# Kernel tuning notes

Hardware: AMD Instinct MI355X
Metric: run time of the kernel (lower is better)

The kernel has to match this reference:

```python
import jax, jax.numpy as jnp
import numpy as np

B, L, K, D = 8, 4096, 16, 128


def setup_inputs() -> dict:
    key = jax.random.key(0)
    k1, k2 = jax.random.split(key)
    frame = jax.random.normal(k1, (B, L, 4, 3), dtype=jnp.float32)  # [B,L,4,3]: row0=center, rows1-3=frame axes
    attr = jax.random.normal(k2, (B, L, D), dtype=jnp.float32)
    return {"frame": frame, "attr": attr}


def reference(frame, attr):
    Kmax = 16
    center = frame[:, :, 0]  # [B,L,3]
    # pairwise squared distances (no grad needed through topk selection)
    c_ng = jax.lax.stop_gradient(center)
    diff = c_ng[:, :, None, :] - c_ng[:, None, :, :]  # [B,L,L,3]
    distance_sq = jnp.sum(diff * diff, axis=-1)  # [B,L,L]
    # k nearest neighbors (smallest distance)
    _, nbr = jax.lax.top_k(-distance_sq, Kmax)  # [B,L,K] int32 indices
    # gather neighbor attributes: attr[b, nbr[b,l,k], :]
    gathered_attr = jax.vmap(lambda a, i: a[i])(attr, nbr)  # [B,L,K,D]
    # gather neighbor centers and project delta into local frame
    nbr_center = jax.vmap(lambda c, i: c[i])(center, nbr)  # [B,L,K,3]
    delta = nbr_center - center[:, :, None, :]  # [B,L,K,3]
    euclidian = jnp.einsum('blkc,blcr->blkr', delta, frame[:, :, 1:4])  # [B,L,K,3]
    return (euclidian, gathered_attr)
```

## Files before the change

### kernel.cpp

```cpp
#include <hip/hip_runtime.h>
#include <stdint.h>

typedef unsigned long long u64;
typedef unsigned short u16;
typedef float nfloat4 __attribute__((ext_vector_type(4)));

#define LQ   4096
#define BQ   8
#define KNB  16
#define TPB  512
#define QPB  64
#define BPB  (LQ / QPB)

__device__ __forceinline__ void ceu(uint32_t &a, uint32_t &b) {
    const uint32_t mn = a < b ? a : b;
    const uint32_t mx = a < b ? b : a;
    a = mn; b = mx;
}
__device__ __forceinline__ void ced(double &a, double &b) {
    const double mn = __builtin_fmin(a, b);
    const double mx = __builtin_fmax(a, b);
    a = mn; b = mx;
}
__device__ __forceinline__ float dist2(float mx, float my, float mz,
                                       float px, float py, float pz) {
    const float dx = __fsub_rn(mx, px);
    const float dy = __fsub_rn(my, py);
    const float dz = __fsub_rn(mz, pz);
    return __fadd_rn(__fadd_rn(__fmul_rn(dx, dx), __fmul_rn(dy, dy)),
                     __fmul_rn(dz, dz));
}

__global__ __launch_bounds__(512) void sort_kernel(
    const float4* __restrict__ frame4,
    float* __restrict__ wx, float* __restrict__ wy,
    float* __restrict__ wz, int* __restrict__ wperm)
{
    __shared__ u64 SK[LQ];
    const int b   = blockIdx.x;
    const int tid = threadIdx.x;
    const float4* fb = frame4 + (size_t)b * LQ * 3;

    for (int j = tid; j < LQ; j += 512) {
        const uint32_t bits = __float_as_uint(fb[j * 3].x);
        const uint32_t mk = (bits & 0x80000000u) ? ~bits : (bits | 0x80000000u);
        SK[j] = ((u64)mk << 32) | (unsigned)j;
    }
    __syncthreads();
    for (int k = 2; k <= LQ; k <<= 1) {
        for (int g = k >> 1; g >= 1; g >>= 1) {
            for (int t = tid; t < LQ / 2; t += 512) {
                const int i  = ((t & ~(g - 1)) << 1) | (t & (g - 1));
                const int j2 = i | g;
                const bool up = ((i & k) == 0);
                const u64 a = SK[i], c = SK[j2];
                if ((a > c) == up) { SK[i] = c; SK[j2] = a; }
            }
            __syncthreads();
        }
    }
    for (int p = tid; p < LQ; p += 512) {
        const int orig = (int)(SK[p] & 0xFFFu);
        const float4 v = fb[orig * 3];
        const size_t o = (size_t)b * LQ + p;
        wx[o] = v.x; wy[o] = v.y; wz[o] = v.z; wperm[o] = orig;
    }
}


__global__ __launch_bounds__(TPB) void knn_fused_kernel(
    const float4* __restrict__ frame4,
    const float4* __restrict__ attr4,
    const float* __restrict__ wx, const float* __restrict__ wy,
    const float* __restrict__ wz, const int* __restrict__ wperm,
    float* __restrict__ out_e,
    nfloat4* __restrict__ outg4)
{
    __shared__ float xs[LQ], ys[LQ], zs[LQ];
    __shared__ u16 perm_lds[LQ];
    __shared__ u16 inv_lds[LQ];
    __shared__ u16 surv[QPB][32];
    __shared__ int nbrs[QPB][KNB];

    const int b    = blockIdx.x >> 6;
    const int qblk = blockIdx.x & (BPB - 1);
    const int tid  = threadIdx.x;

    const float4* fb = frame4 + (size_t)b * LQ * 3;
    {
        const float* bx = wx + (size_t)b * LQ;
        const float* by = wy + (size_t)b * LQ;
        const float* bz = wz + (size_t)b * LQ;
        const int*   bp = wperm + (size_t)b * LQ;
        for (int j = tid; j < LQ; j += TPB) {
            xs[j] = bx[j]; ys[j] = by[j]; zs[j] = bz[j];
            const int pm = bp[j];
            perm_lds[j] = (u16)pm;
            inv_lds[pm] = (u16)j;
        }
    }
    __syncthreads();

    const int qloc = tid >> 3;
    const int h    = tid & 7;
    const int wv   = tid >> 6;
    const int l    = qblk * QPB + qloc;
    const float mx = xs[l], my = ys[l], mz = zs[l];
    const float xq_lo = xs[qblk * QPB + wv * 8];
    const float xq_hi = xs[qblk * QPB + wv * 8 + 7];

    uint32_t R[16];
#pragma unroll
    for (int i = 0; i < 16; ++i) R[i] = 0xFFFFFFFFu;

    const int A = qblk * QPB;
    int lo = A, hi = A;
    bool doneR = false;
    bool doneL = (lo <= 0);

#pragma unroll 1
    while (!(doneR && doneL)) {
        int base;
        {
            bool goRight;
            if (doneR) goRight = false;
            else if (doneL) goRight = true;
            else {
                const float dR = __fsub_rn(xs[hi], xq_hi);
                const float dL = __fsub_rn(xq_lo, xs[lo - 1]);
                goRight = !(dR > dL);
            }
            if (goRight) { base = hi; hi += 64; }
            else         { lo -= 64; base = lo; }
        }
        uint32_t K[8];
#pragma unroll
        for (int s = 0; s < 8; ++s) {
            const int pos = base + s * 8 + h;
            const int pp  = pos < 0 ? 0 : pos;
            const float dx = __fsub_rn(mx, xs[pp]);
            const float dy = __fsub_rn(my, ys[pp]);
            const float dz = __fsub_rn(mz, zs[pp]);
            const float d  = __fmaf_rn(dz, dz, __fmaf_rn(dy, dy, __fmul_rn(dx, dx)));
            const uint32_t key = (__float_as_uint(d) & 0xFFFFF000u) | (unsigned)pos;
            K[s] = (pos >= 0) ? key : 0xFFFFFFFFu;
        }
        ceu(K[0],K[1]); ceu(K[2],K[3]); ceu(K[4],K[5]); ceu(K[6],K[7]);
        ceu(K[0],K[2]); ceu(K[1],K[3]); ceu(K[4],K[6]); ceu(K[5],K[7]);
        ceu(K[1],K[2]); ceu(K[5],K[6]);
        ceu(K[0],K[4]); ceu(K[1],K[5]); ceu(K[2],K[6]); ceu(K[3],K[7]);
        ceu(K[2],K[4]); ceu(K[3],K[5]);
        ceu(K[1],K[2]); ceu(K[3],K[4]); ceu(K[5],K[6]);
#pragma unroll
        for (int t = 0; t < 8; ++t) {
            const uint32_t x = R[8 + t], y = K[7 - t];
            R[8 + t] = x < y ? x : y;
        }
#pragma unroll
        for (int g = 8; g >= 1; g >>= 1)
#pragma unroll
            for (int i = 0; i < 16; ++i)
                if ((i & g) == 0) ceu(R[i], R[i + g]);

        uint32_t ub = R[15] | 0xFFFu;
        { uint32_t t;
          t = __shfl_xor(ub, 1, 64); ub = ub < t ? ub : t;
          t = __shfl_xor(ub, 2, 64); ub = ub < t ? ub : t;
          t = __shfl_xor(ub, 4, 64); ub = ub < t ? ub : t; }
        uint32_t ubb = (ub & 0xFFFFF000u) | 0xFFFu;
        ubb = ubb >> 12;
        ubb = (ubb << 12) | 0xFFFu;
        ubb = (ubb > 0xFFFFFFEFu) ? 0xFFFFFFFFu : ubb + 16u;

        if (!doneR) {
            if (hi >= LQ) doneR = true;
            else {
                const float dxm = __fsub_rn(xs[hi], mx);
                const bool st = (dxm > 0.f) &&
                                (__float_as_uint(__fmul_rn(dxm, dxm)) > ubb);
                if (__all(st)) doneR = true;
            }
        }
        if (!doneL) {
            if (lo <= 0) doneL = true;
            else {
                const float dxm = __fsub_rn(mx, xs[lo - 1]);
                const bool st = (dxm > 0.f) &&
                                (__float_as_uint(__fmul_rn(dxm, dxm)) > ubb);
                if (__all(st)) doneL = true;
            }
        }
    }

    {
        uint32_t P[16];
#pragma unroll
        for (int i = 0; i < 16; ++i) P[i] = __shfl_xor(R[i], 1, 64);
        const bool lo1 = (h & 1) == 0;
#pragma unroll
        for (int i = 0; i < 16; ++i) {
            const uint32_t o = P[15 - i];
            R[i] = lo1 ? (R[i] < o ? R[i] : o) : (R[i] > o ? R[i] : o);
        }
#pragma unroll
        for (int g = 8; g >= 1; g >>= 1)
#pragma unroll
            for (int i = 0; i < 16; ++i)
                if ((i & g) == 0) ceu(R[i], R[i + g]);
    }
    {
        uint32_t P[16];
#pragma unroll
        for (int i = 0; i < 16; ++i) P[i] = __shfl_xor(R[i], 3, 64);
        const bool lo2 = (h & 2) == 0;
#pragma unroll
        for (int i = 0; i < 16; ++i) {
            const uint32_t o = P[15 - i];
            R[i] = lo2 ? (R[i] < o ? R[i] : o) : (R[i] > o ? R[i] : o);
        }
#pragma unroll
        for (int i = 0; i < 16; ++i) P[i] = __shfl_xor(R[i], 1, 64);
        const bool lo1 = (h & 1) == 0;
#pragma unroll
        for (int i = 0; i < 16; ++i) {
            const uint32_t o = P[i];
            R[i] = lo1 ? (R[i] < o ? R[i] : o) : (R[i] > o ? R[i] : o);
        }
#pragma unroll
        for (int g = 8; g >= 1; g >>= 1)
#pragma unroll
            for (int i = 0; i < 16; ++i)
                if ((i & g) == 0) ceu(R[i], R[i + g]);
    }
    {
        uint32_t P[16];
#pragma unroll
        for (int i = 0; i < 16; ++i) P[i] = __shfl_xor(R[i], 7, 64);
        const bool lo4 = (h & 4) == 0;
#pragma unroll
        for (int i = 0; i < 16; ++i) {
            const uint32_t o = P[15 - i];
            R[i] = lo4 ? (R[i] < o ? R[i] : o) : (R[i] > o ? R[i] : o);
        }
#pragma unroll
        for (int i = 0; i < 16; ++i) P[i] = __shfl_xor(R[i], 2, 64);
        const bool lo2 = (h & 2) == 0;
#pragma unroll
        for (int i = 0; i < 16; ++i) {
            const uint32_t o = P[i];
            R[i] = lo2 ? (R[i] < o ? R[i] : o) : (R[i] > o ? R[i] : o);
        }
#pragma unroll
        for (int i = 0; i < 16; ++i) P[i] = __shfl_xor(R[i], 1, 64);
        const bool lo1 = (h & 1) == 0;
#pragma unroll
        for (int i = 0; i < 16; ++i) {
            const uint32_t o = P[i];
            R[i] = lo1 ? (R[i] < o ? R[i] : o) : (R[i] > o ? R[i] : o);
        }
#pragma unroll
        for (int g = 8; g >= 1; g >>= 1)
#pragma unroll
            for (int i = 0; i < 16; ++i)
                if ((i & g) == 0) ceu(R[i], R[i + g]);
    }

    if (h < 2) {
#pragma unroll
        for (int i = 0; i < 16; ++i)
            surv[qloc][h * 16 + i] = (u16)(R[i] & 0xFFFu);
    }

    double kd[4];
#pragma unroll
    for (int s = 0; s < 4; ++s) {
        const int sp = surv[qloc][h * 4 + s];
        const float d = dist2(mx, my, mz, xs[sp], ys[sp], zs[sp]);
        kd[s] = __builtin_bit_cast(double,
                 ((u64)__float_as_uint(d) << 12) | (unsigned)perm_lds[sp]);
    }
    ced(kd[0],kd[1]); ced(kd[2],kd[3]); ced(kd[0],kd[2]); ced(kd[1],kd[3]); ced(kd[1],kd[2]);
    {
        double P[4];
#pragma unroll
        for (int s = 0; s < 4; ++s) P[s] = __shfl_xor(kd[s], 1, 64);
        const bool lo1 = (h & 1) == 0;
#pragma unroll
        for (int s = 0; s < 4; ++s) {
            const double o = P[3 - s];
            kd[s] = lo1 ? __builtin_fmin(kd[s], o) : __builtin_fmax(kd[s], o);
        }
        ced(kd[0],kd[2]); ced(kd[1],kd[3]); ced(kd[0],kd[1]); ced(kd[2],kd[3]);
    }
    {
        double P[4];
#pragma unroll
        for (int s = 0; s < 4; ++s) P[s] = __shfl_xor(kd[s], 3, 64);
        const bool lo2 = (h & 2) == 0;
#pragma unroll
        for (int s = 0; s < 4; ++s) {
            const double o = P[3 - s];
            kd[s] = lo2 ? __builtin_fmin(kd[s], o) : __builtin_fmax(kd[s], o);
        }
#pragma unroll
        for (int s = 0; s < 4; ++s) P[s] = __shfl_xor(kd[s], 1, 64);
        const bool lo1 = (h & 1) == 0;
#pragma unroll
        for (int s = 0; s < 4; ++s) {
            const double o = P[s];
            kd[s] = lo1 ? __builtin_fmin(kd[s], o) : __builtin_fmax(kd[s], o);
        }
        ced(kd[0],kd[2]); ced(kd[1],kd[3]); ced(kd[0],kd[1]); ced(kd[2],kd[3]);
    }
    {
        double P[4];
#pragma unroll
        for (int s = 0; s < 4; ++s) P[s] = __shfl_xor(kd[s], 7, 64);
        const bool lo4 = (h & 4) == 0;
#pragma unroll
        for (int s = 0; s < 4; ++s) {
            const double o = P[3 - s];
            kd[s] = lo4 ? __builtin_fmin(kd[s], o) : __builtin_fmax(kd[s], o);
        }
#pragma unroll
        for (int s = 0; s < 4; ++s) P[s] = __shfl_xor(kd[s], 2, 64);
        const bool lo2 = (h & 2) == 0;
#pragma unroll
        for (int s = 0; s < 4; ++s) {
            const double o = P[s];
            kd[s] = lo2 ? __builtin_fmin(kd[s], o) : __builtin_fmax(kd[s], o);
        }
#pragma unroll
        for (int s = 0; s < 4; ++s) P[s] = __shfl_xor(kd[s], 1, 64);
        const bool lo1 = (h & 1) == 0;
#pragma unroll
        for (int s = 0; s < 4; ++s) {
            const double o = P[s];
            kd[s] = lo1 ? __builtin_fmin(kd[s], o) : __builtin_fmax(kd[s], o);
        }
        ced(kd[0],kd[2]); ced(kd[1],kd[3]); ced(kd[0],kd[1]); ced(kd[2],kd[3]);
    }

    const int ql_orig = perm_lds[l];
    const size_t gq = (size_t)b * LQ + (size_t)ql_orig;
    if (h < 4) {
        const float4 f0 = fb[ql_orig * 3 + 0];
        const float4 f1 = fb[ql_orig * 3 + 1];
        const float4 f2 = fb[ql_orig * 3 + 2];
        const float R00 = f0.w, R01 = f1.x, R02 = f1.y;
        const float R10 = f1.z, R11 = f1.w, R12 = f2.x;
        const float R20 = f2.y, R21 = f2.z, R22 = f2.w;
        float e[12];
#pragma unroll
        for (int s = 0; s < 4; ++s) {
            const u64 bits = __builtin_bit_cast(u64, kd[s]);
            const int jo = (int)(bits & 0xFFFu);
            nbrs[qloc][h * 4 + s] = jo;
            const int sp = inv_lds[jo];
            const float dx = xs[sp] - mx;
            const float dy = ys[sp] - my;
            const float dz = zs[sp] - mz;
            e[s * 3 + 0] = dx * R00 + dy * R10 + dz * R20;
            e[s * 3 + 1] = dx * R01 + dy * R11 + dz * R21;
            e[s * 3 + 2] = dx * R02 + dy * R12 + dz * R22;
        }
        float4* eo = (float4*)(out_e + gq * 48 + h * 12);
        float4 v0 = {e[0], e[1], e[2],  e[3]};
        float4 v1 = {e[4], e[5], e[6],  e[7]};
        float4 v2 = {e[8], e[9], e[10], e[11]};
        eo[0] = v0; eo[1] = v1; eo[2] = v2;
    }

    const float4* ab = attr4 + (((size_t)b) << 12) * 32;
    const int lane = tid & 63;
    const int qbase = qblk * QPB + wv * 8;
#pragma unroll 4
    for (int it = 0; it < 64; ++it) {
        const int idx = it * 64 + lane;
        const int qw  = idx >> 9;
        const int r   = idx & 511;
        const int k   = r >> 5, d4 = r & 31;
        const int nb  = nbrs[wv * 8 + qw][k];
        const int qo  = perm_lds[qbase + qw];
        const float4 v = ab[(size_t)nb * 32 + d4];
        nfloat4 nv = {v.x, v.y, v.z, v.w};
        __builtin_nontemporal_store(nv,
            &outg4[((size_t)b * LQ + (size_t)qo) * 512 + r]);
    }
}

extern "C" void kernel_launch(void* const* d_in, const int* in_sizes, int n_in,
                              void* d_out, int out_size, void* d_ws, size_t ws_size,
                              hipStream_t stream)
{
    const float* frame = (const float*)d_in[0];
    const float* attr  = (const float*)d_in[1];
    float* out = (float*)d_out;

    float* wxp = (float*)d_ws;
    float* wyp = wxp + BQ * LQ;
    float* wzp = wyp + BQ * LQ;
    int*   wpp = (int*)(wzp + BQ * LQ);

    sort_kernel<<<BQ, 512, 0, stream>>>((const float4*)frame, wxp, wyp, wzp, wpp);

    nfloat4* outg4 = (nfloat4*)(out + (size_t)BQ * LQ * KNB * 3);
    knn_fused_kernel<<<BQ * BPB, TPB, 0, stream>>>(
        (const float4*)frame, (const float4*)attr, wxp, wyp, wzp, wpp,
        out, outg4);
}
```

Baseline: 396.8 us.

## Replace adaptive bidirectional kNN scan with seeded radius bound and binary-searched window

New measurement: 372.5 us. 6.1% less time.

```diff
diff --git a/kernel.cpp b/kernel.cpp
--- a/kernel.cpp
+++ b/kernel.cpp
@@ -106,44 +106,21 @@
     const int wv   = tid >> 6;
     const int l    = qblk * QPB + qloc;
     const float mx = xs[l], my = ys[l], mz = zs[l];
-    const float xq_lo = xs[qblk * QPB + wv * 8];
-    const float xq_hi = xs[qblk * QPB + wv * 8 + 7];
 
     uint32_t R[16];
 #pragma unroll
     for (int i = 0; i < 16; ++i) R[i] = 0xFFFFFFFFu;
 
-    const int A = qblk * QPB;
-    int lo = A, hi = A;
-    bool doneR = false;
-    bool doneL = (lo <= 0);
-
-#pragma unroll 1
-    while (!(doneR && doneL)) {
-        int base;
-        {
-            bool goRight;
-            if (doneR) goRight = false;
-            else if (doneL) goRight = true;
-            else {
-                const float dR = __fsub_rn(xs[hi], xq_hi);
-                const float dL = __fsub_rn(xq_lo, xs[lo - 1]);
-                goRight = !(dR > dL);
-            }
-            if (goRight) { base = hi; hi += 64; }
-            else         { lo -= 64; base = lo; }
-        }
+    auto scan_group = [&](const int base) {
         uint32_t K[8];
 #pragma unroll
         for (int s = 0; s < 8; ++s) {
             const int pos = base + s * 8 + h;
-            const int pp  = pos < 0 ? 0 : pos;
-            const float dx = __fsub_rn(mx, xs[pp]);
-            const float dy = __fsub_rn(my, ys[pp]);
-            const float dz = __fsub_rn(mz, zs[pp]);
+            const float dx = __fsub_rn(mx, xs[pos]);
+            const float dy = __fsub_rn(my, ys[pos]);
+            const float dz = __fsub_rn(mz, zs[pos]);
             const float d  = __fmaf_rn(dz, dz, __fmaf_rn(dy, dy, __fmul_rn(dx, dx)));
-            const uint32_t key = (__float_as_uint(d) & 0xFFFFF000u) | (unsigned)pos;
-            K[s] = (pos >= 0) ? key : 0xFFFFFFFFu;
+            K[s] = (__float_as_uint(d) & 0xFFFFF000u) | (unsigned)pos;
         }
         ceu(K[0],K[1]); ceu(K[2],K[3]); ceu(K[4],K[5]); ceu(K[6],K[7]);
         ceu(K[0],K[2]); ceu(K[1],K[3]); ceu(K[4],K[6]); ceu(K[5],K[7]);
@@ -161,109 +138,126 @@
 #pragma unroll
             for (int i = 0; i < 16; ++i)
                 if ((i & g) == 0) ceu(R[i], R[i + g]);
-
-        uint32_t ub = R[15] | 0xFFFu;
-        { uint32_t t;
-          t = __shfl_xor(ub, 1, 64); ub = ub < t ? ub : t;
-          t = __shfl_xor(ub, 2, 64); ub = ub < t ? ub : t;
-          t = __shfl_xor(ub, 4, 64); ub = ub < t ? ub : t; }
-        uint32_t ubb = (ub & 0xFFFFF000u) | 0xFFFu;
-        ubb = ubb >> 12;
-        ubb = (ubb << 12) | 0xFFFu;
-        ubb = (ubb > 0xFFFFFFEFu) ? 0xFFFFFFFFu : ubb + 16u;
-
-        if (!doneR) {
-            if (hi >= LQ) doneR = true;
-            else {
-                const float dxm = __fsub_rn(xs[hi], mx);
-                const bool st = (dxm > 0.f) &&
-                                (__float_as_uint(__fmul_rn(dxm, dxm)) > ubb);
-                if (__all(st)) doneR = true;
-            }
-        }
-        if (!doneL) {
-            if (lo <= 0) doneL = true;
-            else {
-                const float dxm = __fsub_rn(mx, xs[lo - 1]);
-                const bool st = (dxm > 0.f) &&
-                                (__float_as_uint(__fmul_rn(dxm, dxm)) > ubb);
-                if (__all(st)) doneL = true;
-            }
-        }
-    }
-
-    {
-        uint32_t P[16];
-#pragma unroll
-        for (int i = 0; i < 16; ++i) P[i] = __shfl_xor(R[i], 1, 64);
-        const bool lo1 = (h & 1) == 0;
-#pragma unroll
-        for (int i = 0; i < 16; ++i) {
-            const uint32_t o = P[15 - i];
-            R[i] = lo1 ? (R[i] < o ? R[i] : o) : (R[i] > o ? R[i] : o);
-        }
-#pragma unroll
-        for (int g = 8; g >= 1; g >>= 1)
-#pragma unroll
-            for (int i = 0; i < 16; ++i)
-                if ((i & g) == 0) ceu(R[i], R[i + g]);
-    }
-    {
-        uint32_t P[16];
-#pragma unroll
-        for (int i = 0; i < 16; ++i) P[i] = __shfl_xor(R[i], 3, 64);
-        const bool lo2 = (h & 2) == 0;
-#pragma unroll
-        for (int i = 0; i < 16; ++i) {
-            const uint32_t o = P[15 - i];
-            R[i] = lo2 ? (R[i] < o ? R[i] : o) : (R[i] > o ? R[i] : o);
-        }
-#pragma unroll
-        for (int i = 0; i < 16; ++i) P[i] = __shfl_xor(R[i], 1, 64);
-        const bool lo1 = (h & 1) == 0;
-#pragma unroll
-        for (int i = 0; i < 16; ++i) {
-            const uint32_t o = P[i];
-            R[i] = lo1 ? (R[i] < o ? R[i] : o) : (R[i] > o ? R[i] : o);
-        }
-#pragma unroll
-        for (int g = 8; g >= 1; g >>= 1)
-#pragma unroll
-            for (int i = 0; i < 16; ++i)
-                if ((i & g) == 0) ceu(R[i], R[i + g]);
-    }
-    {
-        uint32_t P[16];
-#pragma unroll
-        for (int i = 0; i < 16; ++i) P[i] = __shfl_xor(R[i], 7, 64);
-        const bool lo4 = (h & 4) == 0;
-#pragma unroll
-        for (int i = 0; i < 16; ++i) {
-            const uint32_t o = P[15 - i];
-            R[i] = lo4 ? (R[i] < o ? R[i] : o) : (R[i] > o ? R[i] : o);
-        }
-#pragma unroll
-        for (int i = 0; i < 16; ++i) P[i] = __shfl_xor(R[i], 2, 64);
-        const bool lo2 = (h & 2) == 0;
-#pragma unroll
-        for (int i = 0; i < 16; ++i) {
-            const uint32_t o = P[i];
-            R[i] = lo2 ? (R[i] < o ? R[i] : o) : (R[i] > o ? R[i] : o);
-        }
-#pragma unroll
-        for (int i = 0; i < 16; ++i) P[i] = __shfl_xor(R[i], 1, 64);
-        const bool lo1 = (h & 1) == 0;
-#pragma unroll
-        for (int i = 0; i < 16; ++i) {
-            const uint32_t o = P[i];
-            R[i] = lo1 ? (R[i] < o ? R[i] : o) : (R[i] > o ? R[i] : o);
-        }
-#pragma unroll
-        for (int g = 8; g >= 1; g >>= 1)
-#pragma unroll
-            for (int i = 0; i < 16; ++i)
-                if ((i & g) == 0) ceu(R[i], R[i + g]);
-    }
+    };
+
+    auto merge128 = [&]() {
+        {
+            uint32_t P[16];
+#pragma unroll
+            for (int i = 0; i < 16; ++i) P[i] = __shfl_xor(R[i], 1, 64);
+            const bool lo1 = (h & 1) == 0;
+#pragma unroll
+            for (int i = 0; i < 16; ++i) {
+                const uint32_t o = P[15 - i];
+                R[i] = lo1 ? (R[i] < o ? R[i] : o) : (R[i] > o ? R[i] : o);
+            }
+#pragma unroll
+            for (int g = 8; g >= 1; g >>= 1)
+#pragma unroll
+                for (int i = 0; i < 16; ++i)
+                    if ((i & g) == 0) ceu(R[i], R[i + g]);
+        }
+        {
+            uint32_t P[16];
+#pragma unroll
+            for (int i = 0; i < 16; ++i) P[i] = __shfl_xor(R[i], 3, 64);
+            const bool lo2 = (h & 2) == 0;
+#pragma unroll
+            for (int i = 0; i < 16; ++i) {
+                const uint32_t o = P[15 - i];
+                R[i] = lo2 ? (R[i] < o ? R[i] : o) : (R[i] > o ? R[i] : o);
+            }
+#pragma unroll
+            for (int i = 0; i < 16; ++i) P[i] = __shfl_xor(R[i], 1, 64);
+            const bool lo1 = (h & 1) == 0;
+#pragma unroll
+            for (int i = 0; i < 16; ++i) {
+                const uint32_t o = P[i];
+                R[i] = lo1 ? (R[i] < o ? R[i] : o) : (R[i] > o ? R[i] : o);
+            }
+#pragma unroll
+            for (int g = 8; g >= 1; g >>= 1)
+#pragma unroll
+                for (int i = 0; i < 16; ++i)
+                    if ((i & g) == 0) ceu(R[i], R[i + g]);
+        }
+        {
+            uint32_t P[16];
+#pragma unroll
+            for (int i = 0; i < 16; ++i) P[i] = __shfl_xor(R[i], 7, 64);
+            const bool lo4 = (h & 4) == 0;
+#pragma unroll
+            for (int i = 0; i < 16; ++i) {
+                const uint32_t o = P[15 - i];
+                R[i] = lo4 ? (R[i] < o ? R[i] : o) : (R[i] > o ? R[i] : o);
+            }
+#pragma unroll
+            for (int i = 0; i < 16; ++i) P[i] = __shfl_xor(R[i], 2, 64);
+            const bool lo2 = (h & 2) == 0;
+#pragma unroll
+            for (int i = 0; i < 16; ++i) {
+                const uint32_t o = P[i];
+                R[i] = lo2 ? (R[i] < o ? R[i] : o) : (R[i] > o ? R[i] : o);
+            }
+#pragma unroll
+            for (int i = 0; i < 16; ++i) P[i] = __shfl_xor(R[i], 1, 64);
+            const bool lo1 = (h & 1) == 0;
+#pragma unroll
+            for (int i = 0; i < 16; ++i) {
+                const uint32_t o = P[i];
+                R[i] = lo1 ? (R[i] < o ? R[i] : o) : (R[i] > o ? R[i] : o);
+            }
+#pragma unroll
+            for (int g = 8; g >= 1; g >>= 1)
+#pragma unroll
+                for (int i = 0; i < 16; ++i)
+                    if ((i & g) == 0) ceu(R[i], R[i + g]);
+        }
+    };
+
+    const int A = qblk * QPB;
+    int seedLo = A - 64;
+    if (seedLo < 0) seedLo = 0;
+    if (seedLo > LQ - 192) seedLo = LQ - 192;
+    scan_group(seedLo); scan_group(seedLo + 64); scan_group(seedLo + 128);
+    merge128();
+
+    const uint32_t ub16 = __shfl(R[15], (tid & 63) & ~7, 64);
+    uint32_t ubb = (ub16 | 0xFFFu) >> 12;
+    ubb = (ubb << 12) | 0xFFFu;
+    ubb = (ubb > 0xFFFFFFEFu) ? 0xFFFFFFFFu : ubb + 16u;
+
+    float rq = __fsqrt_rn(__uint_as_float(ubb));
+    rq = __uint_as_float(__float_as_uint(rq) + 8);
+
+    float xloN = __fsub_rn(mx, rq);
+    float xhiN = __fadd_rn(mx, rq);
+    { float t;
+      t = __shfl_xor(xloN,  8, 64); xloN = fminf(xloN, t);
+      t = __shfl_xor(xloN, 16, 64); xloN = fminf(xloN, t);
+      t = __shfl_xor(xloN, 32, 64); xloN = fminf(xloN, t);
+      t = __shfl_xor(xhiN,  8, 64); xhiN = fmaxf(xhiN, t);
+      t = __shfl_xor(xhiN, 16, 64); xhiN = fmaxf(xhiN, t);
+      t = __shfl_xor(xhiN, 32, 64); xhiN = fmaxf(xhiN, t); }
+
+    int loP = 0, hiP = 0;
+#pragma unroll 1
+    for (int st = 2048; st >= 1; st >>= 1) {
+        if (loP + st <= LQ && xs[loP + st - 1] <  xloN) loP += st;
+        if (hiP + st <= LQ && xs[hiP + st - 1] <= xhiN) hiP += st;
+    }
+    const int loGrp = loP & ~63;
+    const int hiGrp = (hiP + 63) & ~63;
+
+    const int e1 = (hiGrp < seedLo) ? hiGrp : seedLo;
+#pragma unroll 1
+    for (int base = loGrp; base < e1; base += 64) scan_group(base);
+    const int sHi = seedLo + 192;
+    const int b2 = (loGrp > sHi) ? loGrp : sHi;
+#pragma unroll 1
+    for (int base = b2; base < hiGrp; base += 64) scan_group(base);
+
+    merge128();
 
     if (h < 2) {
 #pragma unroll
```
